# Optimization experiments

Measured on AMD Instinct MI355X. Metric: run time of the kernel, lower is better.

The kernel has to match this reference:

```python
import jax, jax.numpy as jnp
import numpy as np

N, E, R = 50000, 800000, 3
IN_DIM, HID, HEADS = 128, 128, 4
C = HID // HEADS  # per-head channels = 32
NEG_SLOPE = 0.2   # GATConv default LeakyReLU slope
LN_EPS = 1e-5


def setup_inputs() -> dict:
    key = jax.random.key(0)
    ks = jax.random.split(key, 8)
    x = jax.random.normal(ks[0], (N, IN_DIM), jnp.float32)
    edge_index = jax.random.randint(ks[1], (R, 2, E), 0, N, jnp.int32)
    edge_attr = jax.random.uniform(ks[2], (R, E, 1), dtype=jnp.float32)  # unused by GATConv (edge_dim=None)
    W = jax.random.normal(ks[3], (R, IN_DIM, HID), jnp.float32) / np.float32(np.sqrt(IN_DIM))
    att_src = jax.random.normal(ks[4], (R, HEADS, C), jnp.float32) / np.float32(np.sqrt(C))
    att_dst = jax.random.normal(ks[5], (R, HEADS, C), jnp.float32) / np.float32(np.sqrt(C))
    bias = jnp.zeros((R, HID), jnp.float32)
    gate = jnp.ones((R,), jnp.float32)
    ln_gamma = jnp.ones((HID,), jnp.float32)
    ln_beta = jnp.zeros((HID,), jnp.float32)
    return dict(x=x, edge_index=edge_index, edge_attr=edge_attr, W=W,
                att_src=att_src, att_dst=att_dst, bias=bias, gate=gate,
                ln_gamma=ln_gamma, ln_beta=ln_beta)


def _gat(x, W, a_src, a_dst, b, ei):
    # One GATConv (concat heads, no self loops, eval-mode so no attn dropout).
    h = (x @ W).reshape(N, HEADS, C)                      # [N,H,C]
    alpha_src = jnp.einsum('nhc,hc->nh', h, a_src)        # [N,H]
    alpha_dst = jnp.einsum('nhc,hc->nh', h, a_dst)        # [N,H]
    src, dst = ei[0], ei[1]
    e = jax.nn.leaky_relu(alpha_src[src] + alpha_dst[dst], NEG_SLOPE)  # [E,H]
    # segment-softmax over incoming edges of each dst node
    e_max = jax.ops.segment_max(e, dst, num_segments=N)   # [N,H] (-inf for isolated nodes, never indexed)
    e_exp = jnp.exp(e - e_max[dst])                       # [E,H]
    denom = jax.ops.segment_sum(e_exp, dst, num_segments=N)
    alpha = e_exp / (denom[dst] + 1e-16)                  # [E,H]
    msg = h[src] * alpha[:, :, None]                      # [E,H,C] edge gather + weight
    out = jax.ops.segment_sum(msg, dst, num_segments=N)   # [N,H,C] scatter-aggregate
    return out.reshape(N, HID) + b


def reference(x, edge_index, edge_attr, W, att_src, att_dst, bias, gate, ln_gamma, ln_beta):
    # edge_attr is accepted but unused: GATConv was built without edge_dim.
    outs = jax.vmap(_gat, in_axes=(None, 0, 0, 0, 0, 0))(x, W, att_src, att_dst, bias, edge_index)  # [R,N,HID]
    gw = jax.nn.softmax(gate)                             # gated fusion weights [R]
    h = jnp.einsum('r,rnd->nd', gw, outs)                 # [N,HID]
    h = h + x                                             # rescale = Identity (in_dim == hid)
    mu = jnp.mean(h, axis=-1, keepdims=True)
    var = jnp.var(h, axis=-1, keepdims=True)
    h = (h - mu) / jnp.sqrt(var + LN_EPS) * ln_gamma + ln_beta
    return h, gw  # dropout is identity in eval mode
```

## Files before the change

### kernel.cpp

```cpp
#include <hip/hip_runtime.h>

#define N_NODES 50000
#define E_EDGES 800000
#define R_REL 3
#define HID 128
#define HEADS 4
#define CAP 64
#define NPART 64
#define PSIZE 782
#define CHUNKS_A 98
#define CAP_A 224

typedef __attribute__((ext_vector_type(8))) short short8;
typedef __attribute__((ext_vector_type(4))) float float4v;

__device__ __forceinline__ unsigned short f2bf(float f) {
    unsigned int u = __float_as_uint(f);
    u += 0x7fffu + ((u >> 16) & 1u);
    return (unsigned short)(u >> 16);
}
__device__ __forceinline__ float bf_lo(unsigned int u) { return __uint_as_float(u << 16); }
__device__ __forceinline__ float bf_hi(unsigned int u) { return __uint_as_float(u & 0xffff0000u); }

#define WCONV_T (R_REL * HID * HID)
#define SETUP_BLKS 193
#define FILLA_BLKS (R_REL * CHUNKS_A)
__global__ __launch_bounds__(256) void setup_fillA_kernel(const float* __restrict__ W,
                                                          const float* __restrict__ gate,
                                                          const int* __restrict__ edge_idx,
                                                          unsigned short* __restrict__ wtb,
                                                          float* __restrict__ gw_out,
                                                          unsigned* __restrict__ regions,
                                                          int* __restrict__ bc) {
    __shared__ unsigned buf[NPART * CAP_A];
    __shared__ int lcnt[NPART];
    int bid = blockIdx.x;
    if (bid < SETUP_BLKS) {
        int tid = bid * 256 + threadIdx.x;
        if (tid < WCONV_T) {
            int r = tid >> 14, rem = tid & 16383, n = rem >> 7, k = rem & 127;
            wtb[tid] = f2bf(W[r * 16384 + k * 128 + n]);
        } else if (tid == WCONV_T) {
            float g0 = gate[0], g1 = gate[1], g2 = gate[2];
            float mg = fmaxf(g0, fmaxf(g1, g2));
            float e0 = __expf(g0 - mg), e1 = __expf(g1 - mg), e2 = __expf(g2 - mg);
            float inv = 1.f / (e0 + e1 + e2);
            gw_out[0] = e0 * inv; gw_out[1] = e1 * inv; gw_out[2] = e2 * inv;
        }
        return;
    }
    int fb = bid - SETUP_BLKS;
    int r = fb / CHUNKS_A, c = fb % CHUNKS_A;
    if (threadIdx.x < NPART) lcnt[threadIdx.x] = 0;
    __syncthreads();
    const int4* s4 = (const int4*)(edge_idx + (long)r * 2 * E_EDGES);
    const int4* d4 = (const int4*)(edge_idx + (long)r * 2 * E_EDGES + E_EDGES);
    int i0 = c * 2048;
    int i1 = i0 + 2048; if (i1 > E_EDGES / 4) i1 = E_EDGES / 4;
    for (int i = i0 + threadIdx.x; i < i1; i += 256) {
        int4 sv = s4[i];
        int4 dv = d4[i];
#pragma unroll
        for (int j = 0; j < 4; ++j) {
            int dst = (j == 0) ? dv.x : (j == 1) ? dv.y : (j == 2) ? dv.z : dv.w;
            int src = (j == 0) ? sv.x : (j == 1) ? sv.y : (j == 2) ? sv.z : sv.w;
            int p = dst / PSIZE;
            int reldst = dst - p * PSIZE;
            int pos = atomicAdd(&lcnt[p], 1);
            if (pos < CAP_A) buf[p * CAP_A + pos] = ((unsigned)reldst << 16) | (unsigned)src;
        }
    }
    __syncthreads();
    long rbase = (long)(r * CHUNKS_A + c) * NPART;
    int wv = threadIdx.x >> 6, ln = threadIdx.x & 63;
    for (int p = wv; p < NPART; p += 4) {
        int n = lcnt[p]; if (n > CAP_A) n = CAP_A;
        unsigned* dp = regions + (rbase + p) * CAP_A;
        for (int i = ln; i < n; i += 64) dp[i] = buf[p * CAP_A + i];
    }
    if (threadIdx.x < NPART) {
        int n = lcnt[threadIdx.x]; if (n > CAP_A) n = CAP_A;
        bc[rbase + threadIdx.x] = n;
    }
}

#define FILLB_BLKS (R_REL * NPART)
#define STRIPS 3125
#define BLK_PER_REL 782
#define GEMM_BLKS (R_REL * BLK_PER_REL)
__global__ __launch_bounds__(256) void gemm_fillB_kernel(const float* __restrict__ x,
                                                         const unsigned short* __restrict__ wtb,
                                                         unsigned short* __restrict__ hb,
                                                         const float* __restrict__ att_src,
                                                         const float* __restrict__ att_dst,
                                                         float* __restrict__ asrc,
                                                         float* __restrict__ adst,
                                                         const unsigned* __restrict__ regions,
                                                         const int* __restrict__ bc,
                                                         int* __restrict__ cnt,
                                                         unsigned short* __restrict__ slots) {
    __shared__ int lc[PSIZE];
    int bid = blockIdx.x;
    if (bid < FILLB_BLKS) {
        int r = bid / NPART, p = bid % NPART;
        int base = p * PSIZE;
        int psz = N_NODES - base; if (psz > PSIZE) psz = PSIZE;
        if (psz < 0) psz = 0;
        for (int i = threadIdx.x; i < PSIZE; i += 256) lc[i] = 0;
        __syncthreads();
        int wv = threadIdx.x >> 6, ln = threadIdx.x & 63;
        for (int c = wv; c < CHUNKS_A; c += 4) {
            long rb = (long)(r * CHUNKS_A + c) * NPART + p;
            int n = bc[rb];
            const unsigned* sp = regions + rb * CAP_A;
            for (int i = ln; i < n; i += 64) {
                unsigned e = sp[i];
                int reldst = e >> 16;
                int src = e & 0xffff;
                int pos = atomicAdd(&lc[reldst], 1);
                if (pos < CAP)
                    slots[((long)(r * N_NODES + base + reldst)) * CAP + pos] = (unsigned short)src;
            }
        }
        __syncthreads();
        for (int i = threadIdx.x; i < psz; i += 256)
            cnt[r * N_NODES + base + i] = lc[i];
        return;
    }
    int gb = bid - FILLB_BLKS;
    int r = gb / BLK_PER_REL;
    int sb = gb % BLK_PER_REL;
    int strip = sb * 4 + (threadIdx.x >> 6);
    if (strip >= STRIPS) return;
    int lane = threadIdx.x & 63;
    int m = lane & 15, quad = lane >> 4;

    const float* xrow = x + (long)(strip * 16 + m) * HID + quad * 8;
    short8 B[4];
#pragma unroll
    for (int kc = 0; kc < 4; ++kc) {
        float4 f0 = *(const float4*)(xrow + kc * 32);
        float4 f1 = *(const float4*)(xrow + kc * 32 + 4);
        short8 b;
        b[0] = (short)f2bf(f0.x); b[1] = (short)f2bf(f0.y);
        b[2] = (short)f2bf(f0.z); b[3] = (short)f2bf(f0.w);
        b[4] = (short)f2bf(f1.x); b[5] = (short)f2bf(f1.y);
        b[6] = (short)f2bf(f1.z); b[7] = (short)f2bf(f1.w);
        B[kc] = b;
    }

    const unsigned short* wt = wtb + r * HID * HID;
    float4v acc[8];
#pragma unroll
    for (int cb = 0; cb < 8; ++cb) acc[cb] = (float4v){0.f, 0.f, 0.f, 0.f};
#pragma unroll
    for (int cb = 0; cb < 8; ++cb) {
        const unsigned short* wrow = wt + (cb * 16 + m) * HID + quad * 8;
#pragma unroll
        for (int kc = 0; kc < 4; ++kc) {
            short8 A = *(const short8*)(wrow + kc * 32);
            acc[cb] = __builtin_amdgcn_mfma_f32_16x16x32_bf16(A, B[kc], acc[cb], 0, 0, 0);
        }
    }
    int node = strip * 16 + m;
    unsigned short* hrow = hb + ((long)r * N_NODES + node) * HID;
#pragma unroll
    for (int cb = 0; cb < 8; ++cb) {
        uint2 o;
        o.x = f2bf(acc[cb][0]) | ((unsigned)f2bf(acc[cb][1]) << 16);
        o.y = f2bf(acc[cb][2]) | ((unsigned)f2bf(acc[cb][3]) << 16);
        *(uint2*)(hrow + cb * 16 + quad * 4) = o;
    }
    const float* ar = att_src + r * HID;
    const float* dr = att_dst + r * HID;
    float sa[4] = {0.f, 0.f, 0.f, 0.f}, sd[4] = {0.f, 0.f, 0.f, 0.f};
#pragma unroll
    for (int cb = 0; cb < 8; ++cb) {
        int hd = cb >> 1;
#pragma unroll
        for (int i = 0; i < 4; ++i) {
            int c = cb * 16 + quad * 4 + i;
            sa[hd] += acc[cb][i] * ar[c];
            sd[hd] += acc[cb][i] * dr[c];
        }
    }
#pragma unroll
    for (int hd = 0; hd < 4; ++hd) {
        sa[hd] += __shfl_xor(sa[hd], 16, 64); sa[hd] += __shfl_xor(sa[hd], 32, 64);
        sd[hd] += __shfl_xor(sd[hd], 16, 64); sd[hd] += __shfl_xor(sd[hd], 32, 64);
    }
    float wa = quad == 0 ? sa[0] : quad == 1 ? sa[1] : quad == 2 ? sa[2] : sa[3];
    float wd = quad == 0 ? sd[0] : quad == 1 ? sd[1] : quad == 2 ? sd[2] : sd[3];
    asrc[((long)r * N_NODES + node) * 4 + quad] = wa;
    adst[((long)r * N_NODES + node) * 4 + quad] = wd;
}

__global__ __launch_bounds__(256) void aggr_kernel(const unsigned short* __restrict__ hb,
                                                   const int* __restrict__ cnt,
                                                   const unsigned short* __restrict__ slots,
                                                   const float* __restrict__ asrc,
                                                   const float* __restrict__ adst,
                                                   const float* __restrict__ gate,
                                                   const float* __restrict__ x,
                                                   const float* __restrict__ bias,
                                                   const float* __restrict__ ln_g,
                                                   const float* __restrict__ ln_b,
                                                   float* __restrict__ out) {
    int node = blockIdx.x * 4 + (threadIdx.x >> 6);
    int lane = threadIdx.x & 63;
    int q = lane >> 4;
    int l = lane & 15;
    int hd = l >> 2;

    float4 xv0 = ((const float4*)x)[(long)node * 32 + 2 * l];
    float4 xv1 = ((const float4*)x)[(long)node * 32 + 2 * l + 1];

    float g0 = gate[0], g1 = gate[1], g2 = gate[2];
    float mg = fmaxf(g0, fmaxf(g1, g2));
    float ge0 = __expf(g0 - mg), ge1 = __expf(g1 - mg), ge2 = __expf(g2 - mg);
    float ginv = 1.f / (ge0 + ge1 + ge2);
    float gw0 = ge0 * ginv, gw1 = ge1 * ginv, gw2 = ge2 * ginv;

    int d0 = cnt[node];
    int d1 = cnt[N_NODES + node];
    int d2 = cnt[2 * N_NODES + node];
    int deg0 = d0 < CAP ? d0 : CAP;
    int deg1 = d1 < CAP ? d1 : CAP;
    int deg2 = d2 < CAP ? d2 : CAP;
    const unsigned short* slb0 = slots + (long)node * CAP;
    const unsigned short* slb1 = slots + (long)(N_NODES + node) * CAP;
    const unsigned short* slb2 = slots + (long)(2 * N_NODES + node) * CAP;
    const uint2* slp0 = (const uint2*)slb0;
    const uint2* slp1 = (const uint2*)slb1;
    const uint2* slp2 = (const uint2*)slb2;
    uint2 PA00 = slp0[q],     PA10 = slp1[q],     PA20 = slp2[q];
    uint2 PA01 = slp0[q + 4], PA11 = slp1[q + 4], PA21 = slp2[q + 4];
    int fb0 = deg0 > 0 ? (int)slb0[0] : 0;
    int fb1 = deg1 > 0 ? (int)slb1[0] : 0;
    int fb2 = deg2 > 0 ? (int)slb2[0] : 0;
    float av0 = adst[(long)node * 4 + hd];
    float av1 = adst[((long)N_NODES + node) * 4 + hd];
    float av2 = adst[((long)2 * N_NODES + node) * 4 + hd];

    float A0_0 = 0.f, A0_1 = 0.f, A0_2 = 0.f, A0_3 = 0.f, A0_4 = 0.f, A0_5 = 0.f, A0_6 = 0.f, A0_7 = 0.f;
    float A1_0 = 0.f, A1_1 = 0.f, A1_2 = 0.f, A1_3 = 0.f, A1_4 = 0.f, A1_5 = 0.f, A1_6 = 0.f, A1_7 = 0.f;
    float A2_0 = 0.f, A2_1 = 0.f, A2_2 = 0.f, A2_3 = 0.f, A2_4 = 0.f, A2_5 = 0.f, A2_6 = 0.f, A2_7 = 0.f;
    float DEN0 = 0.f, DEN1 = 0.f, DEN2 = 0.f;

    int dmax = deg0 > deg1 ? deg0 : deg1; if (deg2 > dmax) dmax = deg2;

#define DECL_LOAD(r, P)                                                                    \
    bool v##r##_0 = sb     < deg##r, v##r##_1 = sb + 1 < deg##r,                           \
         v##r##_2 = sb + 2 < deg##r, v##r##_3 = sb + 3 < deg##r;                           \
    int s##r##_0 = v##r##_0 ? (int)((P).x & 0xffffu) : fb##r;                              \
    int s##r##_1 = v##r##_1 ? (int)((P).x >> 16)     : fb##r;                              \
    int s##r##_2 = v##r##_2 ? (int)((P).y & 0xffffu) : fb##r;                              \
    int s##r##_3 = v##r##_3 ? (int)((P).y >> 16)     : fb##r;                              \
    uint4 u##r##_0 = ((const uint4*)(hb + ((long)(r) * N_NODES + s##r##_0) * HID))[l];     \
    uint4 u##r##_1 = ((const uint4*)(hb + ((long)(r) * N_NODES + s##r##_1) * HID))[l];     \
    uint4 u##r##_2 = ((const uint4*)(hb + ((long)(r) * N_NODES + s##r##_2) * HID))[l];     \
    uint4 u##r##_3 = ((const uint4*)(hb + ((long)(r) * N_NODES + s##r##_3) * HID))[l];     \
    float w##r##_0 = asrc[((long)(r) * N_NODES + s##r##_0) * 4 + hd];                      \
    float w##r##_1 = asrc[((long)(r) * N_NODES + s##r##_1) * 4 + hd];                      \
    float w##r##_2 = asrc[((long)(r) * N_NODES + s##r##_2) * 4 + hd];                      \
    float w##r##_3 = asrc[((long)(r) * N_NODES + s##r##_3) * 4 + hd];

#define COMPUTE(r)                                                                         \
    {                                                                                      \
    float t0 = w##r##_0 + av##r; t0 = t0 > 0.f ? t0 : 0.2f * t0;                           \
    float t1 = w##r##_1 + av##r; t1 = t1 > 0.f ? t1 : 0.2f * t1;                           \
    float t2 = w##r##_2 + av##r; t2 = t2 > 0.f ? t2 : 0.2f * t2;                           \
    float t3 = w##r##_3 + av##r; t3 = t3 > 0.f ? t3 : 0.2f * t3;                           \
    float e0 = v##r##_0 ? __expf(t0) : 0.f;                                                \
    float e1 = v##r##_1 ? __expf(t1) : 0.f;                                                \
    float e2 = v##r##_2 ? __expf(t2) : 0.f;                                                \
    float e3 = v##r##_3 ? __expf(t3) : 0.f;                                                \
    A##r##_0 += (e0 * bf_lo(u##r##_0.x) + e1 * bf_lo(u##r##_1.x)) + (e2 * bf_lo(u##r##_2.x) + e3 * bf_lo(u##r##_3.x)); \
    A##r##_1 += (e0 * bf_hi(u##r##_0.x) + e1 * bf_hi(u##r##_1.x)) + (e2 * bf_hi(u##r##_2.x) + e3 * bf_hi(u##r##_3.x)); \
    A##r##_2 += (e0 * bf_lo(u##r##_0.y) + e1 * bf_lo(u##r##_1.y)) + (e2 * bf_lo(u##r##_2.y) + e3 * bf_lo(u##r##_3.y)); \
    A##r##_3 += (e0 * bf_hi(u##r##_0.y) + e1 * bf_hi(u##r##_1.y)) + (e2 * bf_hi(u##r##_2.y) + e3 * bf_hi(u##r##_3.y)); \
    A##r##_4 += (e0 * bf_lo(u##r##_0.z) + e1 * bf_lo(u##r##_1.z)) + (e2 * bf_lo(u##r##_2.z) + e3 * bf_lo(u##r##_3.z)); \
    A##r##_5 += (e0 * bf_hi(u##r##_0.z) + e1 * bf_hi(u##r##_1.z)) + (e2 * bf_hi(u##r##_2.z) + e3 * bf_hi(u##r##_3.z)); \
    A##r##_6 += (e0 * bf_lo(u##r##_0.w) + e1 * bf_lo(u##r##_1.w)) + (e2 * bf_lo(u##r##_2.w) + e3 * bf_lo(u##r##_3.w)); \
    A##r##_7 += (e0 * bf_hi(u##r##_0.w) + e1 * bf_hi(u##r##_1.w)) + (e2 * bf_hi(u##r##_2.w) + e3 * bf_hi(u##r##_3.w)); \
    DEN##r += (e0 + e1) + (e2 + e3);                                                       \
    }

#define AGGR_ROUND(kb, P0_, P1_, P2_)                                                      \
    {                                                                                      \
        int sb = (kb) + 4 * q;                                                             \
        DECL_LOAD(0, P0_) DECL_LOAD(1, P1_) DECL_LOAD(2, P2_)                              \
        COMPUTE(0) COMPUTE(1) COMPUTE(2)                                                   \
    }

    if (dmax > 0)  AGGR_ROUND(0,  PA00, PA10, PA20)
    if (dmax > 16) AGGR_ROUND(16, PA01, PA11, PA21)
    if (dmax > 32) {
        uint2 PA02 = slp0[q + 8], PA12 = slp1[q + 8], PA22 = slp2[q + 8];
        AGGR_ROUND(32, PA02, PA12, PA22)
    }
    if (dmax > 48) {
        uint2 PA03 = slp0[q + 12], PA13 = slp1[q + 12], PA23 = slp2[q + 12];
        AGGR_ROUND(48, PA03, PA13, PA23)
    }
#undef AGGR_ROUND
#undef COMPUTE
#undef DECL_LOAD

    float run0 = 0.f, run1 = 0.f, run2 = 0.f, run3 = 0.f;
    float run4 = 0.f, run5 = 0.f, run6 = 0.f, run7 = 0.f;
#define MERGE(r, GW)                                                                       \
    {                                                                                      \
        float a0 = A##r##_0, a1 = A##r##_1, a2 = A##r##_2, a3 = A##r##_3;                  \
        float a4 = A##r##_4, a5 = A##r##_5, a6 = A##r##_6, a7 = A##r##_7;                  \
        float den = DEN##r;                                                                \
        a0 += __shfl_xor(a0, 16, 64); a0 += __shfl_xor(a0, 32, 64);                        \
        a1 += __shfl_xor(a1, 16, 64); a1 += __shfl_xor(a1, 32, 64);                        \
        a2 += __shfl_xor(a2, 16, 64); a2 += __shfl_xor(a2, 32, 64);                        \
        a3 += __shfl_xor(a3, 16, 64); a3 += __shfl_xor(a3, 32, 64);                        \
        a4 += __shfl_xor(a4, 16, 64); a4 += __shfl_xor(a4, 32, 64);                        \
        a5 += __shfl_xor(a5, 16, 64); a5 += __shfl_xor(a5, 32, 64);                        \
        a6 += __shfl_xor(a6, 16, 64); a6 += __shfl_xor(a6, 32, 64);                        \
        a7 += __shfl_xor(a7, 16, 64); a7 += __shfl_xor(a7, 32, 64);                        \
        den += __shfl_xor(den, 16, 64); den += __shfl_xor(den, 32, 64);                    \
        float inv = (GW) / (den + 1e-16f);                                                 \
        run0 += a0 * inv; run1 += a1 * inv; run2 += a2 * inv; run3 += a3 * inv;            \
        run4 += a4 * inv; run5 += a5 * inv; run6 += a6 * inv; run7 += a7 * inv;            \
    }
    MERGE(0, gw0) MERGE(1, gw1) MERGE(2, gw2)
#undef MERGE

    const float4* b4 = (const float4*)bias;
    float4 b00 = b4[2 * l], b01 = b4[2 * l + 1];
    float4 b10 = b4[32 + 2 * l], b11 = b4[32 + 2 * l + 1];
    float4 b20 = b4[64 + 2 * l], b21 = b4[64 + 2 * l + 1];
    float v0 = run0 + xv0.x + gw0 * b00.x + gw1 * b10.x + gw2 * b20.x;
    float v1 = run1 + xv0.y + gw0 * b00.y + gw1 * b10.y + gw2 * b20.y;
    float v2 = run2 + xv0.z + gw0 * b00.z + gw1 * b10.z + gw2 * b20.z;
    float v3 = run3 + xv0.w + gw0 * b00.w + gw1 * b10.w + gw2 * b20.w;
    float v4 = run4 + xv1.x + gw0 * b01.x + gw1 * b11.x + gw2 * b21.x;
    float v5 = run5 + xv1.y + gw0 * b01.y + gw1 * b11.y + gw2 * b21.y;
    float v6 = run6 + xv1.z + gw0 * b01.z + gw1 * b11.z + gw2 * b21.z;
    float v7 = run7 + xv1.w + gw0 * b01.w + gw1 * b11.w + gw2 * b21.w;
    float sum = v0 + v1 + v2 + v3 + v4 + v5 + v6 + v7;
    float sq = v0 * v0 + v1 * v1 + v2 * v2 + v3 * v3 + v4 * v4 + v5 * v5 + v6 * v6 + v7 * v7;
#pragma unroll
    for (int off = 32; off > 0; off >>= 1) {
        sum += __shfl_xor(sum, off, 64);
        sq  += __shfl_xor(sq, off, 64);
    }
    float mean = sum * (1.f / (4 * HID));
    float var = sq * (1.f / (4 * HID)) - mean * mean;
    float rstd = rsqrtf(var + 1e-5f);
    if (q == 0) {
        float4 gv0 = ((const float4*)ln_g)[2 * l], gv1 = ((const float4*)ln_g)[2 * l + 1];
        float4 bv0 = ((const float4*)ln_b)[2 * l], bv1 = ((const float4*)ln_b)[2 * l + 1];
        float4 o0, o1;
        o0.x = (v0 - mean) * rstd * gv0.x + bv0.x;
        o0.y = (v1 - mean) * rstd * gv0.y + bv0.y;
        o0.z = (v2 - mean) * rstd * gv0.z + bv0.z;
        o0.w = (v3 - mean) * rstd * gv0.w + bv0.w;
        o1.x = (v4 - mean) * rstd * gv1.x + bv1.x;
        o1.y = (v5 - mean) * rstd * gv1.y + bv1.y;
        o1.z = (v6 - mean) * rstd * gv1.z + bv1.z;
        o1.w = (v7 - mean) * rstd * gv1.w + bv1.w;
        ((float4*)out)[(long)node * 32 + 2 * l] = o0;
        ((float4*)out)[(long)node * 32 + 2 * l + 1] = o1;
    }
}

extern "C" void kernel_launch(void* const* d_in, const int* in_sizes, int n_in,
                              void* d_out, int out_size, void* d_ws, size_t ws_size,
                              hipStream_t stream) {
    const float* x        = (const float*)d_in[0];
    const int*   edge_idx = (const int*)d_in[1];
    const float* W        = (const float*)d_in[3];
    const float* att_src  = (const float*)d_in[4];
    const float* att_dst  = (const float*)d_in[5];
    const float* bias     = (const float*)d_in[6];
    const float* gate     = (const float*)d_in[7];
    const float* ln_g     = (const float*)d_in[8];
    const float* ln_b     = (const float*)d_in[9];
    float* out = (float*)d_out;

    unsigned short* hb  = (unsigned short*)d_ws;
    float* asrc = (float*)(hb + (long)R_REL * N_NODES * HID);
    float* adst = asrc + R_REL * N_NODES * HEADS;
    int*   cnt  = (int*)(adst + R_REL * N_NODES * HEADS);
    unsigned short* wtb = (unsigned short*)(cnt + R_REL * N_NODES);
    unsigned short* slots = wtb + R_REL * HID * HID;
    unsigned* regions = (unsigned*)(slots + (long)R_REL * N_NODES * CAP);
    int* bc = (int*)(regions + (long)R_REL * CHUNKS_A * NPART * CAP_A);

    setup_fillA_kernel<<<SETUP_BLKS + FILLA_BLKS, 256, 0, stream>>>(
        W, gate, edge_idx, wtb, out + (long)N_NODES * HID, regions, bc);
    gemm_fillB_kernel<<<FILLB_BLKS + GEMM_BLKS, 256, 0, stream>>>(
        x, wtb, hb, att_src, att_dst, asrc, adst, regions, bc, cnt, slots);
    aggr_kernel<<<N_NODES / 4, 256, 0, stream>>>(hb, cnt, slots, asrc, adst, gate,
                                                 x, bias, ln_g, ln_b, out);
}
```

Baseline: 306.4 us.

## Restructure per-relation gather with 8-wide batches and deferred cross-lane reductions

Replaces the lockstep three-relation aggregation rounds, which were bounded by the maximum degree, with per-relation branches sized by each relation's own degree. Degrees of 17 to 32 are handled by an 8-wide gather that issues more loads at once. The cross-lane shuffle reduction is moved after the per-relation scaling, so only the denominators and one combined set of 8 accumulators are shuffled instead of three sets. It also drops the deg>0 guard on the fallback index and uses fmaxf for leaky-relu. The cost is that memory-level parallelism across relations is lost, since each relation's gather now runs in sequence.

```diff
diff --git a/kernel.cpp b/kernel.cpp
--- a/kernel.cpp
+++ b/kernel.cpp
@@ -233,11 +233,10 @@
     const uint2* slp0 = (const uint2*)slb0;
     const uint2* slp1 = (const uint2*)slb1;
     const uint2* slp2 = (const uint2*)slb2;
-    uint2 PA00 = slp0[q],     PA10 = slp1[q],     PA20 = slp2[q];
-    uint2 PA01 = slp0[q + 4], PA11 = slp1[q + 4], PA21 = slp2[q + 4];
-    int fb0 = deg0 > 0 ? (int)slb0[0] : 0;
-    int fb1 = deg1 > 0 ? (int)slb1[0] : 0;
-    int fb2 = deg2 > 0 ? (int)slb2[0] : 0;
+    uint2 Pf0 = slp0[q], Pf1 = slp1[q], Pf2 = slp2[q];
+    int fb0 = (int)slb0[0];
+    int fb1 = (int)slb1[0];
+    int fb2 = (int)slb2[0];
     float av0 = adst[(long)node * 4 + hd];
     float av1 = adst[((long)N_NODES + node) * 4 + hd];
     float av2 = adst[((long)2 * N_NODES + node) * 4 + hd];
@@ -247,88 +246,150 @@
     float A2_0 = 0.f, A2_1 = 0.f, A2_2 = 0.f, A2_3 = 0.f, A2_4 = 0.f, A2_5 = 0.f, A2_6 = 0.f, A2_7 = 0.f;
     float DEN0 = 0.f, DEN1 = 0.f, DEN2 = 0.f;
 
-    int dmax = deg0 > deg1 ? deg0 : deg1; if (deg2 > dmax) dmax = deg2;
-
-#define DECL_LOAD(r, P)                                                                    \
-    bool v##r##_0 = sb     < deg##r, v##r##_1 = sb + 1 < deg##r,                           \
-         v##r##_2 = sb + 2 < deg##r, v##r##_3 = sb + 3 < deg##r;                           \
-    int s##r##_0 = v##r##_0 ? (int)((P).x & 0xffffu) : fb##r;                              \
-    int s##r##_1 = v##r##_1 ? (int)((P).x >> 16)     : fb##r;                              \
-    int s##r##_2 = v##r##_2 ? (int)((P).y & 0xffffu) : fb##r;                              \
-    int s##r##_3 = v##r##_3 ? (int)((P).y >> 16)     : fb##r;                              \
-    uint4 u##r##_0 = ((const uint4*)(hb + ((long)(r) * N_NODES + s##r##_0) * HID))[l];     \
-    uint4 u##r##_1 = ((const uint4*)(hb + ((long)(r) * N_NODES + s##r##_1) * HID))[l];     \
-    uint4 u##r##_2 = ((const uint4*)(hb + ((long)(r) * N_NODES + s##r##_2) * HID))[l];     \
-    uint4 u##r##_3 = ((const uint4*)(hb + ((long)(r) * N_NODES + s##r##_3) * HID))[l];     \
-    float w##r##_0 = asrc[((long)(r) * N_NODES + s##r##_0) * 4 + hd];                      \
-    float w##r##_1 = asrc[((long)(r) * N_NODES + s##r##_1) * 4 + hd];                      \
-    float w##r##_2 = asrc[((long)(r) * N_NODES + s##r##_2) * 4 + hd];                      \
-    float w##r##_3 = asrc[((long)(r) * N_NODES + s##r##_3) * 4 + hd];
-
-#define COMPUTE(r)                                                                         \
-    {                                                                                      \
-    float t0 = w##r##_0 + av##r; t0 = t0 > 0.f ? t0 : 0.2f * t0;                           \
-    float t1 = w##r##_1 + av##r; t1 = t1 > 0.f ? t1 : 0.2f * t1;                           \
-    float t2 = w##r##_2 + av##r; t2 = t2 > 0.f ? t2 : 0.2f * t2;                           \
-    float t3 = w##r##_3 + av##r; t3 = t3 > 0.f ? t3 : 0.2f * t3;                           \
-    float e0 = v##r##_0 ? __expf(t0) : 0.f;                                                \
-    float e1 = v##r##_1 ? __expf(t1) : 0.f;                                                \
-    float e2 = v##r##_2 ? __expf(t2) : 0.f;                                                \
-    float e3 = v##r##_3 ? __expf(t3) : 0.f;                                                \
-    A##r##_0 += (e0 * bf_lo(u##r##_0.x) + e1 * bf_lo(u##r##_1.x)) + (e2 * bf_lo(u##r##_2.x) + e3 * bf_lo(u##r##_3.x)); \
-    A##r##_1 += (e0 * bf_hi(u##r##_0.x) + e1 * bf_hi(u##r##_1.x)) + (e2 * bf_hi(u##r##_2.x) + e3 * bf_hi(u##r##_3.x)); \
-    A##r##_2 += (e0 * bf_lo(u##r##_0.y) + e1 * bf_lo(u##r##_1.y)) + (e2 * bf_lo(u##r##_2.y) + e3 * bf_lo(u##r##_3.y)); \
-    A##r##_3 += (e0 * bf_hi(u##r##_0.y) + e1 * bf_hi(u##r##_1.y)) + (e2 * bf_hi(u##r##_2.y) + e3 * bf_hi(u##r##_3.y)); \
-    A##r##_4 += (e0 * bf_lo(u##r##_0.z) + e1 * bf_lo(u##r##_1.z)) + (e2 * bf_lo(u##r##_2.z) + e3 * bf_lo(u##r##_3.z)); \
-    A##r##_5 += (e0 * bf_hi(u##r##_0.z) + e1 * bf_hi(u##r##_1.z)) + (e2 * bf_hi(u##r##_2.z) + e3 * bf_hi(u##r##_3.z)); \
-    A##r##_6 += (e0 * bf_lo(u##r##_0.w) + e1 * bf_lo(u##r##_1.w)) + (e2 * bf_lo(u##r##_2.w) + e3 * bf_lo(u##r##_3.w)); \
-    A##r##_7 += (e0 * bf_hi(u##r##_0.w) + e1 * bf_hi(u##r##_1.w)) + (e2 * bf_hi(u##r##_2.w) + e3 * bf_hi(u##r##_3.w)); \
-    DEN##r += (e0 + e1) + (e2 + e3);                                                       \
-    }
-
-#define AGGR_ROUND(kb, P0_, P1_, P2_)                                                      \
-    {                                                                                      \
-        int sb = (kb) + 4 * q;                                                             \
-        DECL_LOAD(0, P0_) DECL_LOAD(1, P1_) DECL_LOAD(2, P2_)                              \
-        COMPUTE(0) COMPUTE(1) COMPUTE(2)                                                   \
-    }
-
-    if (dmax > 0)  AGGR_ROUND(0,  PA00, PA10, PA20)
-    if (dmax > 16) AGGR_ROUND(16, PA01, PA11, PA21)
-    if (dmax > 32) {
-        uint2 PA02 = slp0[q + 8], PA12 = slp1[q + 8], PA22 = slp2[q + 8];
-        AGGR_ROUND(32, PA02, PA12, PA22)
-    }
-    if (dmax > 48) {
-        uint2 PA03 = slp0[q + 12], PA13 = slp1[q + 12], PA23 = slp2[q + 12];
-        AGGR_ROUND(48, PA03, PA13, PA23)
-    }
-#undef AGGR_ROUND
-#undef COMPUTE
-#undef DECL_LOAD
-
-    float run0 = 0.f, run1 = 0.f, run2 = 0.f, run3 = 0.f;
-    float run4 = 0.f, run5 = 0.f, run6 = 0.f, run7 = 0.f;
-#define MERGE(r, GW)                                                                       \
-    {                                                                                      \
-        float a0 = A##r##_0, a1 = A##r##_1, a2 = A##r##_2, a3 = A##r##_3;                  \
-        float a4 = A##r##_4, a5 = A##r##_5, a6 = A##r##_6, a7 = A##r##_7;                  \
-        float den = DEN##r;                                                                \
-        a0 += __shfl_xor(a0, 16, 64); a0 += __shfl_xor(a0, 32, 64);                        \
-        a1 += __shfl_xor(a1, 16, 64); a1 += __shfl_xor(a1, 32, 64);                        \
-        a2 += __shfl_xor(a2, 16, 64); a2 += __shfl_xor(a2, 32, 64);                        \
-        a3 += __shfl_xor(a3, 16, 64); a3 += __shfl_xor(a3, 32, 64);                        \
-        a4 += __shfl_xor(a4, 16, 64); a4 += __shfl_xor(a4, 32, 64);                        \
-        a5 += __shfl_xor(a5, 16, 64); a5 += __shfl_xor(a5, 32, 64);                        \
-        a6 += __shfl_xor(a6, 16, 64); a6 += __shfl_xor(a6, 32, 64);                        \
-        a7 += __shfl_xor(a7, 16, 64); a7 += __shfl_xor(a7, 32, 64);                        \
-        den += __shfl_xor(den, 16, 64); den += __shfl_xor(den, 32, 64);                    \
-        float inv = (GW) / (den + 1e-16f);                                                 \
-        run0 += a0 * inv; run1 += a1 * inv; run2 += a2 * inv; run3 += a3 * inv;            \
-        run4 += a4 * inv; run5 += a5 * inv; run6 += a6 * inv; run7 += a7 * inv;            \
-    }
-    MERGE(0, gw0) MERGE(1, gw1) MERGE(2, gw2)
-#undef MERGE
+#define GATHER4(r, P, BASE)                                                               \
+    {                                                                                     \
+        int sb = (BASE) + 4 * q;                                                          \
+        bool b0 = sb < deg##r, b1 = sb + 1 < deg##r, b2 = sb + 2 < deg##r, b3 = sb + 3 < deg##r; \
+        int s0 = b0 ? (int)((P).x & 0xffffu) : fb##r;                                     \
+        int s1 = b1 ? (int)((P).x >> 16) : fb##r;                                         \
+        int s2 = b2 ? (int)((P).y & 0xffffu) : fb##r;                                     \
+        int s3 = b3 ? (int)((P).y >> 16) : fb##r;                                         \
+        const unsigned short* hr = hb + (long)(r) * N_NODES * HID;                        \
+        const float* as = asrc + (long)(r) * N_NODES * 4;                                 \
+        uint4 u0 = ((const uint4*)(hr + (long)s0 * HID))[l];                              \
+        uint4 u1 = ((const uint4*)(hr + (long)s1 * HID))[l];                              \
+        uint4 u2 = ((const uint4*)(hr + (long)s2 * HID))[l];                              \
+        uint4 u3 = ((const uint4*)(hr + (long)s3 * HID))[l];                              \
+        float w0 = as[s0 * 4 + hd], w1 = as[s1 * 4 + hd];                                 \
+        float w2 = as[s2 * 4 + hd], w3 = as[s3 * 4 + hd];                                 \
+        float t0 = w0 + av##r; t0 = fmaxf(t0, 0.2f * t0);                                 \
+        float t1 = w1 + av##r; t1 = fmaxf(t1, 0.2f * t1);                                 \
+        float t2 = w2 + av##r; t2 = fmaxf(t2, 0.2f * t2);                                 \
+        float t3 = w3 + av##r; t3 = fmaxf(t3, 0.2f * t3);                                 \
+        float e0 = b0 ? __expf(t0) : 0.f;                                                 \
+        float e1 = b1 ? __expf(t1) : 0.f;                                                 \
+        float e2 = b2 ? __expf(t2) : 0.f;                                                 \
+        float e3 = b3 ? __expf(t3) : 0.f;                                                 \
+        A##r##_0 += (e0 * bf_lo(u0.x) + e1 * bf_lo(u1.x)) + (e2 * bf_lo(u2.x) + e3 * bf_lo(u3.x)); \
+        A##r##_1 += (e0 * bf_hi(u0.x) + e1 * bf_hi(u1.x)) + (e2 * bf_hi(u2.x) + e3 * bf_hi(u3.x)); \
+        A##r##_2 += (e0 * bf_lo(u0.y) + e1 * bf_lo(u1.y)) + (e2 * bf_lo(u2.y) + e3 * bf_lo(u3.y)); \
+        A##r##_3 += (e0 * bf_hi(u0.y) + e1 * bf_hi(u1.y)) + (e2 * bf_hi(u2.y) + e3 * bf_hi(u3.y)); \
+        A##r##_4 += (e0 * bf_lo(u0.z) + e1 * bf_lo(u1.z)) + (e2 * bf_lo(u2.z) + e3 * bf_lo(u3.z)); \
+        A##r##_5 += (e0 * bf_hi(u0.z) + e1 * bf_hi(u1.z)) + (e2 * bf_hi(u2.z) + e3 * bf_hi(u3.z)); \
+        A##r##_6 += (e0 * bf_lo(u0.w) + e1 * bf_lo(u1.w)) + (e2 * bf_lo(u2.w) + e3 * bf_lo(u3.w)); \
+        A##r##_7 += (e0 * bf_hi(u0.w) + e1 * bf_hi(u1.w)) + (e2 * bf_hi(u2.w) + e3 * bf_hi(u3.w)); \
+        DEN##r += (e0 + e1) + (e2 + e3);                                                  \
+    }
+
+#define GATHER8(r, Pa, Pb)                                                                \
+    {                                                                                     \
+        int sa_ = 4 * q, sb_ = 16 + 4 * q;                                                \
+        bool b0 = sa_ < deg##r, b1 = sa_ + 1 < deg##r, b2 = sa_ + 2 < deg##r, b3 = sa_ + 3 < deg##r; \
+        bool b4 = sb_ < deg##r, b5 = sb_ + 1 < deg##r, b6 = sb_ + 2 < deg##r, b7 = sb_ + 3 < deg##r; \
+        int s0 = b0 ? (int)((Pa).x & 0xffffu) : fb##r;                                    \
+        int s1 = b1 ? (int)((Pa).x >> 16) : fb##r;                                        \
+        int s2 = b2 ? (int)((Pa).y & 0xffffu) : fb##r;                                    \
+        int s3 = b3 ? (int)((Pa).y >> 16) : fb##r;                                        \
+        int s4 = b4 ? (int)((Pb).x & 0xffffu) : fb##r;                                    \
+        int s5 = b5 ? (int)((Pb).x >> 16) : fb##r;                                        \
+        int s6 = b6 ? (int)((Pb).y & 0xffffu) : fb##r;                                    \
+        int s7 = b7 ? (int)((Pb).y >> 16) : fb##r;                                        \
+        const unsigned short* hr = hb + (long)(r) * N_NODES * HID;                        \
+        const float* as = asrc + (long)(r) * N_NODES * 4;                                 \
+        uint4 u0 = ((const uint4*)(hr + (long)s0 * HID))[l];                              \
+        uint4 u1 = ((const uint4*)(hr + (long)s1 * HID))[l];                              \
+        uint4 u2 = ((const uint4*)(hr + (long)s2 * HID))[l];                              \
+        uint4 u3 = ((const uint4*)(hr + (long)s3 * HID))[l];                              \
+        uint4 u4 = ((const uint4*)(hr + (long)s4 * HID))[l];                              \
+        uint4 u5 = ((const uint4*)(hr + (long)s5 * HID))[l];                              \
+        uint4 u6 = ((const uint4*)(hr + (long)s6 * HID))[l];                              \
+        uint4 u7 = ((const uint4*)(hr + (long)s7 * HID))[l];                              \
+        float w0 = as[s0 * 4 + hd], w1 = as[s1 * 4 + hd];                                 \
+        float w2 = as[s2 * 4 + hd], w3 = as[s3 * 4 + hd];                                 \
+        float w4 = as[s4 * 4 + hd], w5 = as[s5 * 4 + hd];                                 \
+        float w6 = as[s6 * 4 + hd], w7 = as[s7 * 4 + hd];                                 \
+        float t0 = w0 + av##r; t0 = fmaxf(t0, 0.2f * t0);                                 \
+        float t1 = w1 + av##r; t1 = fmaxf(t1, 0.2f * t1);                                 \
+        float t2 = w2 + av##r; t2 = fmaxf(t2, 0.2f * t2);                                 \
+        float t3 = w3 + av##r; t3 = fmaxf(t3, 0.2f * t3);                                 \
+        float t4 = w4 + av##r; t4 = fmaxf(t4, 0.2f * t4);                                 \
+        float t5 = w5 + av##r; t5 = fmaxf(t5, 0.2f * t5);                                 \
+        float t6 = w6 + av##r; t6 = fmaxf(t6, 0.2f * t6);                                 \
+        float t7 = w7 + av##r; t7 = fmaxf(t7, 0.2f * t7);                                 \
+        float e0 = b0 ? __expf(t0) : 0.f;                                                 \
+        float e1 = b1 ? __expf(t1) : 0.f;                                                 \
+        float e2 = b2 ? __expf(t2) : 0.f;                                                 \
+        float e3 = b3 ? __expf(t3) : 0.f;                                                 \
+        float e4 = b4 ? __expf(t4) : 0.f;                                                 \
+        float e5 = b5 ? __expf(t5) : 0.f;                                                 \
+        float e6 = b6 ? __expf(t6) : 0.f;                                                 \
+        float e7 = b7 ? __expf(t7) : 0.f;                                                 \
+        A##r##_0 += ((e0 * bf_lo(u0.x) + e1 * bf_lo(u1.x)) + (e2 * bf_lo(u2.x) + e3 * bf_lo(u3.x))) \
+                  + ((e4 * bf_lo(u4.x) + e5 * bf_lo(u5.x)) + (e6 * bf_lo(u6.x) + e7 * bf_lo(u7.x))); \
+        A##r##_1 += ((e0 * bf_hi(u0.x) + e1 * bf_hi(u1.x)) + (e2 * bf_hi(u2.x) + e3 * bf_hi(u3.x))) \
+                  + ((e4 * bf_hi(u4.x) + e5 * bf_hi(u5.x)) + (e6 * bf_hi(u6.x) + e7 * bf_hi(u7.x))); \
+        A##r##_2 += ((e0 * bf_lo(u0.y) + e1 * bf_lo(u1.y)) + (e2 * bf_lo(u2.y) + e3 * bf_lo(u3.y))) \
+                  + ((e4 * bf_lo(u4.y) + e5 * bf_lo(u5.y)) + (e6 * bf_lo(u6.y) + e7 * bf_lo(u7.y))); \
+        A##r##_3 += ((e0 * bf_hi(u0.y) + e1 * bf_hi(u1.y)) + (e2 * bf_hi(u2.y) + e3 * bf_hi(u3.y))) \
+                  + ((e4 * bf_hi(u4.y) + e5 * bf_hi(u5.y)) + (e6 * bf_hi(u6.y) + e7 * bf_hi(u7.y))); \
+        A##r##_4 += ((e0 * bf_lo(u0.z) + e1 * bf_lo(u1.z)) + (e2 * bf_lo(u2.z) + e3 * bf_lo(u3.z))) \
+                  + ((e4 * bf_lo(u4.z) + e5 * bf_lo(u5.z)) + (e6 * bf_lo(u6.z) + e7 * bf_lo(u7.z))); \
+        A##r##_5 += ((e0 * bf_hi(u0.z) + e1 * bf_hi(u1.z)) + (e2 * bf_hi(u2.z) + e3 * bf_hi(u3.z))) \
+                  + ((e4 * bf_hi(u4.z) + e5 * bf_hi(u5.z)) + (e6 * bf_hi(u6.z) + e7 * bf_hi(u7.z))); \
+        A##r##_6 += ((e0 * bf_lo(u0.w) + e1 * bf_lo(u1.w)) + (e2 * bf_lo(u2.w) + e3 * bf_lo(u3.w))) \
+                  + ((e4 * bf_lo(u4.w) + e5 * bf_lo(u5.w)) + (e6 * bf_lo(u6.w) + e7 * bf_lo(u7.w))); \
+        A##r##_7 += ((e0 * bf_hi(u0.w) + e1 * bf_hi(u1.w)) + (e2 * bf_hi(u2.w) + e3 * bf_hi(u3.w))) \
+                  + ((e4 * bf_hi(u4.w) + e5 * bf_hi(u5.w)) + (e6 * bf_hi(u6.w) + e7 * bf_hi(u7.w))); \
+        DEN##r += ((e0 + e1) + (e2 + e3)) + ((e4 + e5) + (e6 + e7));                      \
+    }
+
+#define REL_GATHER(r)                                                                     \
+    if (deg##r > 0) {                                                                     \
+        if (deg##r <= 16) {                                                               \
+            GATHER4(r, Pf##r, 0)                                                          \
+        } else {                                                                          \
+            uint2 Pb_ = slp##r[q + 4];                                                    \
+            GATHER8(r, Pf##r, Pb_)                                                        \
+            if (deg##r > 32) {                                                            \
+                uint2 Pc_ = slp##r[q + 8];                                                \
+                GATHER4(r, Pc_, 32)                                                       \
+                if (deg##r > 48) {                                                        \
+                    uint2 Pd_ = slp##r[q + 12];                                           \
+                    GATHER4(r, Pd_, 48)                                                   \
+                }                                                                         \
+            }                                                                             \
+        }                                                                                 \
+    }
+
+    REL_GATHER(0)
+    REL_GATHER(1)
+    REL_GATHER(2)
+#undef REL_GATHER
+#undef GATHER8
+#undef GATHER4
+
+    DEN0 += __shfl_xor(DEN0, 16, 64); DEN0 += __shfl_xor(DEN0, 32, 64);
+    DEN1 += __shfl_xor(DEN1, 16, 64); DEN1 += __shfl_xor(DEN1, 32, 64);
+    DEN2 += __shfl_xor(DEN2, 16, 64); DEN2 += __shfl_xor(DEN2, 32, 64);
+    float inv0 = gw0 / (DEN0 + 1e-16f);
+    float inv1 = gw1 / (DEN1 + 1e-16f);
+    float inv2 = gw2 / (DEN2 + 1e-16f);
+    float run0 = A0_0 * inv0 + A1_0 * inv1 + A2_0 * inv2;
+    float run1 = A0_1 * inv0 + A1_1 * inv1 + A2_1 * inv2;
+    float run2 = A0_2 * inv0 + A1_2 * inv1 + A2_2 * inv2;
+    float run3 = A0_3 * inv0 + A1_3 * inv1 + A2_3 * inv2;
+    float run4 = A0_4 * inv0 + A1_4 * inv1 + A2_4 * inv2;
+    float run5 = A0_5 * inv0 + A1_5 * inv1 + A2_5 * inv2;
+    float run6 = A0_6 * inv0 + A1_6 * inv1 + A2_6 * inv2;
+    float run7 = A0_7 * inv0 + A1_7 * inv1 + A2_7 * inv2;
+    run0 += __shfl_xor(run0, 16, 64); run0 += __shfl_xor(run0, 32, 64);
+    run1 += __shfl_xor(run1, 16, 64); run1 += __shfl_xor(run1, 32, 64);
+    run2 += __shfl_xor(run2, 16, 64); run2 += __shfl_xor(run2, 32, 64);
+    run3 += __shfl_xor(run3, 16, 64); run3 += __shfl_xor(run3, 32, 64);
+    run4 += __shfl_xor(run4, 16, 64); run4 += __shfl_xor(run4, 32, 64);
+    run5 += __shfl_xor(run5, 16, 64); run5 += __shfl_xor(run5, 32, 64);
+    run6 += __shfl_xor(run6, 16, 64); run6 += __shfl_xor(run6, 32, 64);
+    run7 += __shfl_xor(run7, 16, 64); run7 += __shfl_xor(run7, 32, 64);
 
     const float4* b4 = (const float4*)bias;
     float4 b00 = b4[2 * l], b01 = b4[2 * l + 1];
```

Result: no change. 301.7 us (-1.5%).
